# Performance work log

Hardware: AMD Instinct MI355X
Metric: run time of the kernel (lower is better)

Reference implementation:

```python
import jax, jax.numpy as jnp
import numpy as np

N, L, D, H = 4, 2048, 1024, 16
HD = D // H  # head_dim = 64


def setup_inputs() -> dict:
    key = jax.random.key(0)
    ks = jax.random.split(key, 6)
    x = jax.random.normal(ks[0], (N, L, D), dtype=jnp.float32)
    mask = jax.random.randint(ks[1], (N, L), 0, 2).astype(bool)
    W_qkv = jax.random.normal(ks[2], (3 * D, D), dtype=jnp.float32) * (1.0 / np.sqrt(D))
    b_qkv = jax.random.normal(ks[3], (3 * D,), dtype=jnp.float32) * 0.02
    W_out = jax.random.normal(ks[4], (D, D), dtype=jnp.float32) * (1.0 / np.sqrt(D))
    b_out = jax.random.normal(ks[5], (D,), dtype=jnp.float32) * 0.02
    return {"x": x, "mask": mask, "W_qkv": W_qkv, "b_qkv": b_qkv,
            "W_out": W_out, "b_out": b_out}


def reference(x, mask, W_qkv, b_qkv, W_out, b_out):
    # qkv projection: torch Linear is y = x @ W.T + b
    qkv = jnp.einsum('nld,ed->nle', x, W_qkv) + b_qkv          # [N, L, 3D]
    q, k, v = jnp.split(qkv, 3, axis=-1)                        # each [N, L, D]
    # [N, L, D] -> [N, H, L, HD]
    to_heads = lambda t: t.reshape(N, L, H, HD).transpose(0, 2, 1, 3)
    q, k, v = to_heads(q), to_heads(k), to_heads(v)
    scale = 1.0 / np.sqrt(HD)
    scores = jnp.einsum('nhqd,nhkd->nhqk', q, k) * scale        # [N, H, L, L]
    # faithful to source: masked_fill where mask is True -> -1e9
    scores = jnp.where(mask[:, None, None, :], -1e9, scores)
    attn = jax.nn.softmax(scores, axis=-1)                      # dropout = identity (eval)
    out = jnp.einsum('nhqk,nhkd->nhqd', attn, v)                # [N, H, L, HD]
    out = out.transpose(0, 2, 1, 3).reshape(N, L, D)
    return jnp.einsum('nld,ed->nle', out, W_out) + b_out
```

## Files before the change

### kernel.cpp

```cpp
#include <hip/hip_runtime.h>
#include <hip/hip_bf16.h>
#include <cmath>

#define NB   4
#define LL   2048
#define DD   1024
#define HH   16
#define HD   64

typedef __bf16 bf16;
typedef __bf16 bf16x4 __attribute__((ext_vector_type(4)));
typedef __bf16 bf16x8 __attribute__((ext_vector_type(8)));
typedef float  f32x4  __attribute__((ext_vector_type(4)));
typedef float  f32x8  __attribute__((ext_vector_type(8)));

__device__ __forceinline__ void gload16(void* lds_base, const void* gsrc) {
    __builtin_amdgcn_global_load_lds(
        (const __attribute__((address_space(1))) unsigned int*)gsrc,
        (__attribute__((address_space(3))) unsigned int*)lds_base, 16, 0, 0);
}

__global__ __launch_bounds__(1024) void mask_prep(const unsigned char* __restrict__ mraw,
                                                  float* __restrict__ maskB) {
    __shared__ int anyOdd;
    if (threadIdx.x == 0) anyOdd = 0;
    __syncthreads();
    const int base = blockIdx.x * 1024;
    const int i = base + threadIdx.x;
    if ((i & 3) != 0 && mraw[i] != 0) atomicOr(&anyOdd, 1);
    __syncthreads();
    const bool isBytes = (anyOdd != 0);
    int v = isBytes ? (int)mraw[i] : ((const int*)mraw)[i];
    maskB[i] = v ? -1.4426950408889634e9f : -12.0f;
}

__global__ __launch_bounds__(256) void cast_f32_bf16(const float* __restrict__ src,
                                                     bf16* __restrict__ dst, int n8) {
    const int i = blockIdx.x * 256 + threadIdx.x;
    if (i >= n8) return;
    const float4* s = (const float4*)src + (size_t)i * 2;
    float4 a = s[0], b = s[1];
    bf16x8 o;
    o[0] = (bf16)a.x; o[1] = (bf16)a.y; o[2] = (bf16)a.z; o[3] = (bf16)a.w;
    o[4] = (bf16)b.x; o[5] = (bf16)b.y; o[6] = (bf16)b.z; o[7] = (bf16)b.w;
    *((bf16x8*)dst + i) = o;
}

template <int EPI>
__global__ __launch_bounds__(256) void gemm_mfma(const bf16* __restrict__ A,
                                                 const bf16* __restrict__ B,
                                                 const float* __restrict__ bias,
                                                 void* __restrict__ C0v,
                                                 void* __restrict__ C1v,
                                                 void* __restrict__ C2v,
                                                 int M, int N, int K) {
    __shared__ __attribute__((aligned(16))) char As0[8192];
    __shared__ __attribute__((aligned(16))) char As1[8192];
    __shared__ __attribute__((aligned(16))) char Bs0[8192];
    __shared__ __attribute__((aligned(16))) char Bs1[8192];

    const int tid = threadIdx.x;
    const int wave = tid >> 6;
    const int lane = tid & 63;
    const int kl = lane & 15;
    const int h = lane >> 4;
    const int wm = wave >> 1;
    const int wn = wave & 1;
    const int m0 = blockIdx.y * 128;
    const int n0 = blockIdx.x * 128;

    f32x4 acc[4][4];
#pragma unroll
    for (int i = 0; i < 4; ++i)
#pragma unroll
        for (int j = 0; j < 4; ++j) acc[i][j] = (f32x4){0.f, 0.f, 0.f, 0.f};

    const int sr = wave * 16 + (lane >> 2);
    const int sc = (lane & 3) * 16;
    const char* A0 = (const char*)A + ((size_t)(m0 + sr) * K) * 2 + sc;
    const char* A1 = (const char*)A + ((size_t)(m0 + 64 + sr) * K) * 2 + sc;
    const char* B0 = (const char*)B + ((size_t)(n0 + sr) * K) * 2 + sc;
    const char* B1 = (const char*)B + ((size_t)(n0 + 64 + sr) * K) * 2 + sc;
    const int wofs = wave * 1024;

#define GSTAGE(AS, BS, kt)                          \
    do {                                            \
        gload16((AS) + wofs,        A0 + (kt) * 2); \
        gload16((AS) + wofs + 4096, A1 + (kt) * 2); \
        gload16((BS) + wofs,        B0 + (kt) * 2); \
        gload16((BS) + wofs + 4096, B1 + (kt) * 2); \
    } while (0)

#define GCOMPUTE(AS, BS)                                                           \
    do {                                                                           \
        bf16x8 a[4], b[4];                                                         \
        _Pragma("unroll") for (int mt = 0; mt < 4; ++mt)                           \
            a[mt] = *(const bf16x8*)((AS) + (wm * 64 + mt * 16 + kl) * 64 + h * 16); \
        _Pragma("unroll") for (int nt = 0; nt < 4; ++nt)                           \
            b[nt] = *(const bf16x8*)((BS) + (wn * 64 + nt * 16 + kl) * 64 + h * 16); \
        _Pragma("unroll") for (int mt = 0; mt < 4; ++mt)                           \
            _Pragma("unroll") for (int nt = 0; nt < 4; ++nt)                       \
                acc[mt][nt] = __builtin_amdgcn_mfma_f32_16x16x32_bf16(             \
                    a[mt], b[nt], acc[mt][nt], 0, 0, 0);                           \
    } while (0)

    GSTAGE(As0, Bs0, 0);
    asm volatile("s_waitcnt vmcnt(0)" ::: "memory");
    __builtin_amdgcn_s_barrier();

    for (int t = 0; t < 32; t += 2) {
        GSTAGE(As1, Bs1, (t + 1) * 32);
        __builtin_amdgcn_sched_barrier(0);
        GCOMPUTE(As0, Bs0);
        asm volatile("s_waitcnt vmcnt(0)" ::: "memory");
        __builtin_amdgcn_s_barrier();
        if (t + 2 < 32) {
            GSTAGE(As0, Bs0, (t + 2) * 32);
            __builtin_amdgcn_sched_barrier(0);
            GCOMPUTE(As1, Bs1);
            asm volatile("s_waitcnt vmcnt(0)" ::: "memory");
            __builtin_amdgcn_s_barrier();
        } else {
            GCOMPUTE(As1, Bs1);
        }
    }
#undef GSTAGE
#undef GCOMPUTE

    if (EPI == 1) {
        float* C0 = (float*)C0v;
#pragma unroll
        for (int mt = 0; mt < 4; ++mt) {
            const int mb = m0 + wm * 64 + mt * 16 + 4 * h;
#pragma unroll
            for (int nt = 0; nt < 4; ++nt) {
                const int n = n0 + wn * 64 + nt * 16 + kl;
                const float bv = bias[n];
#pragma unroll
                for (int r = 0; r < 4; ++r)
                    C0[(size_t)(mb + r) * N + n] = acc[mt][nt][r] + bv;
            }
        }
    } else {
        const int which = n0 >> 10;
        if (which < 2) {
            bf16* dst = (which == 0) ? (bf16*)C0v : (bf16*)C1v;
#pragma unroll
            for (int mt = 0; mt < 4; ++mt) {
                const int mb = m0 + wm * 64 + mt * 16 + 4 * h;
#pragma unroll
                for (int nt = 0; nt < 4; ++nt) {
                    const int gn = n0 + wn * 64 + nt * 16 + kl;
                    const float bv = bias[gn];
                    const int nn = gn & 1023;
                    const int hh = nn >> 6;
                    const int d = nn & 63;
#pragma unroll
                    for (int r = 0; r < 4; ++r) {
                        const int m = mb + r;
                        const int n_ = m >> 11;
                        const int l_ = m & 2047;
                        dst[((size_t)(n_ * HH + hh) * LL + l_) * HD + d] = (bf16)(acc[mt][nt][r] + bv);
                    }
                }
            }
        } else {
            bf16* dst = (bf16*)C2v;
#pragma unroll
            for (int mt = 0; mt < 4; ++mt) {
                const int mb = m0 + wm * 64 + mt * 16 + 4 * h;
                const int n_ = mb >> 11;
                const int l0 = mb & 2047;
#pragma unroll
                for (int nt = 0; nt < 4; ++nt) {
                    const int gn = n0 + wn * 64 + nt * 16 + kl;
                    const float bv = bias[gn];
                    const int nn = gn & 1023;
                    const int hh = nn >> 6;
                    const int d = nn & 63;
                    bf16x4 o4;
#pragma unroll
                    for (int r = 0; r < 4; ++r) o4[r] = (bf16)(acc[mt][nt][r] + bv);
                    *(bf16x4*)(dst + ((size_t)(n_ * HH + hh) * HD + d) * LL + l0) = o4;
                }
            }
        }
    }
}

#define SWZ3(row) ((((row) & 3) | ((((row) >> 3) & 1) << 2)) << 4)

__global__ __launch_bounds__(512) void attn_mfma(const bf16* __restrict__ Qg,
                                                 const bf16* __restrict__ Kg,
                                                 const bf16* __restrict__ VTg,
                                                 const float* __restrict__ maskB,
                                                 bf16* __restrict__ Oout) {
    __shared__ __attribute__((aligned(16))) char KtB0[8192];
    __shared__ __attribute__((aligned(16))) char KtB1[8192];
    __shared__ __attribute__((aligned(16))) char VtB0[8192];
    __shared__ __attribute__((aligned(16))) char VtB1[8192];

    const int tid = threadIdx.x;
    const int wave = tid >> 6;
    const int lane = tid & 63;
    const int kl = lane & 15;
    const int h = lane >> 4;

    const int f = blockIdx.x;
    const int qb = (f >> 3) & 7;
    const int bh = (f & 7) | ((f >> 6) << 3);
    const int n_ = bh >> 4;
    const int hh = bh & 15;
    const int q0 = qb * 256 + wave * 32;

    bf16x8 qf[2][2];
#pragma unroll
    for (int qt = 0; qt < 2; ++qt)
#pragma unroll
        for (int st = 0; st < 2; ++st)
            qf[qt][st] = *(const bf16x8*)(Qg + (((size_t)bh * LL + q0 + qt * 16 + kl) * HD + st * 32 + h * 8));

    f32x4 Oa[2][4];
    f32x4 Osum[2];
#pragma unroll
    for (int qt = 0; qt < 2; ++qt) {
        Osum[qt] = (f32x4){0.f, 0.f, 0.f, 0.f};
#pragma unroll
        for (int t = 0; t < 4; ++t) Oa[qt][t] = (f32x4){0.f, 0.f, 0.f, 0.f};
    }

    bf16x8 ones;
#pragma unroll
    for (int j = 0; j < 8; ++j) ones[j] = (bf16)1.0f;

    int koff[2][2][2];
#pragma unroll
    for (int c = 0; c < 2; ++c) {
        const int r1 = c * 32 + ((kl >> 2) << 3) + (kl & 3);
        const int r2 = r1 + 4;
#pragma unroll
        for (int st = 0; st < 2; ++st) {
            koff[c][0][st] = r1 * 128 + ((st * 64 + h * 16) ^ SWZ3(r1));
            koff[c][1][st] = r2 * 128 + ((st * 64 + h * 16) ^ SWZ3(r2));
        }
    }
    int voff[2][4];
#pragma unroll
    for (int c = 0; c < 2; ++c)
#pragma unroll
        for (int tt = 0; tt < 4; ++tt) {
            const int row = tt * 16 + kl;
            voff[c][tt] = row * 128 + ((c * 64 + h * 16) ^ SWZ3(row));
        }

    const int rA = wave * 8 + (lane >> 3);
    const int swA = ((lane & 7) << 4) ^ SWZ3(rA);
    const char* Kb = (const char*)Kg + (size_t)bh * LL * 128;
    const char* Vb = (const char*)VTg + (size_t)bh * HD * (LL * 2);
    const char* kSA = Kb + (size_t)rA * 128 + swA;
    const char* vSA = Vb + (size_t)rA * 4096 + swA;

    const float* mptr = maskB + n_ * LL + h * 8;
    const float scale = 0.18033688011f;

#define STAGE_TO(KT, VT, k0s)                                   \
    do {                                                        \
        gload16((KT) + wave * 1024, kSA + (size_t)(k0s) * 128); \
        gload16((VT) + wave * 1024, vSA + (k0s) * 2);           \
    } while (0)

#define LOADMK(MK, k0s)                                                      \
    do {                                                                     \
        _Pragma("unroll") for (int c = 0; c < 2; ++c)                        \
            _Pragma("unroll") for (int f2 = 0; f2 < 2; ++f2)                 \
                MK[c][f2] = *(const f32x4*)(mptr + (k0s) + c * 32 + f2 * 4); \
    } while (0)

#define COMPUTE(KT, VT, MK)                                                            \
    do {                                                                               \
        bf16x8 kf[2][2][2], vf[2][4];                                                  \
        _Pragma("unroll") for (int c = 0; c < 2; ++c)                                  \
            _Pragma("unroll") for (int fr = 0; fr < 2; ++fr)                           \
                _Pragma("unroll") for (int st = 0; st < 2; ++st)                       \
                    kf[c][fr][st] = *(const bf16x8*)((KT) + koff[c][fr][st]);          \
        __builtin_amdgcn_sched_barrier(0);             \
        _Pragma("unroll") for (int c = 0; c < 2; ++c)                                  \
            _Pragma("unroll") for (int tt = 0; tt < 4; ++tt)                           \
                vf[c][tt] = *(const bf16x8*)((VT) + voff[c][tt]);                      \
        asm volatile("s_waitcnt lgkmcnt(8)" ::: "memory");                \
        __builtin_amdgcn_sched_barrier(0);                                             \
        bf16x8 pa[2][2];                                                               \
        _Pragma("unroll") for (int qt = 0; qt < 2; ++qt) {                             \
            f32x4 sv[2][2];                                                            \
            _Pragma("unroll") for (int c = 0; c < 2; ++c)                              \
                _Pragma("unroll") for (int fr = 0; fr < 2; ++fr) {                     \
                    f32x4 z = {0.f, 0.f, 0.f, 0.f};                                    \
                    f32x4 a = __builtin_amdgcn_mfma_f32_16x16x32_bf16(kf[c][fr][0],    \
                                                         qf[qt][0], z, 0, 0, 0);       \
                    sv[c][fr] = __builtin_amdgcn_mfma_f32_16x16x32_bf16(kf[c][fr][1],  \
                                                         qf[qt][1], a, 0, 0, 0);       \
                }                                                                      \
            _Pragma("unroll") for (int c = 0; c < 2; ++c) {                            \
                f32x8 pf;                                                              \
                _Pragma("unroll") for (int f2 = 0; f2 < 2; ++f2) {                     \
                    f32x4 s = sv[c][f2] * scale + MK[c][f2];                           \
                    _Pragma("unroll") for (int r = 0; r < 4; ++r)                      \
                        pf[f2 * 4 + r] = __builtin_amdgcn_exp2f(s[r]);                 \
                }                                                                      \
                pa[qt][c] = __builtin_convertvector(pf, bf16x8);                       \
            }                                                                          \
        }                                                                              \
        asm volatile("s_waitcnt lgkmcnt(0)" ::: "memory");                \
        __builtin_amdgcn_sched_barrier(0);                                             \
        _Pragma("unroll") for (int qt = 0; qt < 2; ++qt) {                             \
            Osum[qt] = __builtin_amdgcn_mfma_f32_16x16x32_bf16(pa[qt][0], ones,        \
                                                               Osum[qt], 0, 0, 0);     \
            Osum[qt] = __builtin_amdgcn_mfma_f32_16x16x32_bf16(pa[qt][1], ones,        \
                                                               Osum[qt], 0, 0, 0);     \
            _Pragma("unroll") for (int c = 0; c < 2; ++c)                              \
                _Pragma("unroll") for (int tt = 0; tt < 4; ++tt)                       \
                    Oa[qt][tt] = __builtin_amdgcn_mfma_f32_16x16x32_bf16(pa[qt][c],    \
                                                 vf[c][tt], Oa[qt][tt], 0, 0, 0);      \
        }                                                                              \
    } while (0)

    f32x4 mkA[2][2], mkB[2][2];

    LOADMK(mkA, 0);
    STAGE_TO(KtB0, VtB0, 0);
    asm volatile("s_waitcnt vmcnt(0)" ::: "memory");
    __builtin_amdgcn_s_barrier();

    for (int t = 0; t < 32; t += 2) {
        STAGE_TO(KtB1, VtB1, (t + 1) * 64);
        __builtin_amdgcn_sched_barrier(0);
        LOADMK(mkB, (t + 1) * 64);
        COMPUTE(KtB0, VtB0, mkA);
        asm volatile("s_waitcnt vmcnt(4)" ::: "memory");
        __builtin_amdgcn_s_barrier();

        if (t + 2 < 32) {
            STAGE_TO(KtB0, VtB0, (t + 2) * 64);
            __builtin_amdgcn_sched_barrier(0);
            LOADMK(mkA, (t + 2) * 64);
            COMPUTE(KtB1, VtB1, mkB);
            asm volatile("s_waitcnt vmcnt(4)" ::: "memory");
            __builtin_amdgcn_s_barrier();
        } else {
            COMPUTE(KtB1, VtB1, mkB);
        }
    }

#pragma unroll
    for (int qt = 0; qt < 2; ++qt) {
#pragma unroll
        for (int r = 0; r < 4; ++r) {
            const float inv = 1.0f / Osum[qt][r];
            const int qrow = q0 + qt * 16 + h * 4 + r;
#pragma unroll
            for (int tt = 0; tt < 4; ++tt)
                Oout[((size_t)n_ * LL + qrow) * DD + hh * HD + tt * 16 + kl] =
                    (bf16)(Oa[qt][tt][r] * inv);
        }
    }
#undef STAGE_TO
#undef LOADMK
#undef COMPUTE
}

extern "C" void kernel_launch(void* const* d_in, const int* in_sizes, int n_in,
                              void* d_out, int out_size, void* d_ws, size_t ws_size,
                              hipStream_t stream) {
    const float* x     = (const float*)d_in[0];
    const void*  mask  = d_in[1];
    const float* W_qkv = (const float*)d_in[2];
    const float* b_qkv = (const float*)d_in[3];
    const float* W_out = (const float*)d_in[4];
    const float* b_out = (const float*)d_in[5];
    float* out = (float*)d_out;

    char* ws = (char*)d_ws;
    float* maskB = (float*)ws;
    bf16*  xb    = (bf16*)(ws + (1ull  << 20));
    bf16*  wqb   = (bf16*)(ws + (18ull << 20));
    bf16*  wob   = (bf16*)(ws + (25ull << 20));
    bf16*  qb    = (bf16*)(ws + (28ull << 20));
    bf16*  kb    = (bf16*)(ws + (45ull << 20));
    bf16*  vtb   = (bf16*)(ws + (62ull << 20));
    bf16*  attnb = (bf16*)(ws + (79ull << 20));

    mask_prep<<<8, 1024, 0, stream>>>((const unsigned char*)mask, maskB);

    cast_f32_bf16<<<(NB * LL * DD / 8) / 256, 256, 0, stream>>>(x, xb, NB * LL * DD / 8);
    cast_f32_bf16<<<(3 * DD * DD / 8) / 256, 256, 0, stream>>>(W_qkv, wqb, 3 * DD * DD / 8);
    cast_f32_bf16<<<(DD * DD / 8) / 256, 256, 0, stream>>>(W_out, wob, DD * DD / 8);

    gemm_mfma<0><<<dim3(3 * DD / 128, NB * LL / 128), 256, 0, stream>>>(
        xb, wqb, b_qkv, qb, kb, vtb, NB * LL, 3 * DD, DD);

    attn_mfma<<<512, 512, 0, stream>>>(qb, kb, vtb, maskB, attnb);

    gemm_mfma<1><<<dim3(DD / 128, NB * LL / 128), 256, 0, stream>>>(
        attnb, wob, b_out, out, nullptr, nullptr, NB * LL, DD, DD);
}
```

Baseline: 202.9 us.

## Load attention K/V fragments directly from global memory instead of LDS staging

Removes the double-buffered LDS staging of K and V tiles, along with its async global-to-LDS loads, swizzled offsets and per-tile block barriers. Each wave now reads its K/V MFMA fragments and mask values straight from global memory every iteration. This drops the synchronisation and LDS traffic, but each of the 8 waves in a block now fetches the same K/V tile on its own. Those uncoalesced, redundant global/L2 reads can leave the MFMA pipeline waiting on memory.

```diff
diff --git a/kernel.cpp b/kernel.cpp
--- a/kernel.cpp
+++ b/kernel.cpp
@@ -188,18 +188,11 @@
     }
 }
 
-#define SWZ3(row) ((((row) & 3) | ((((row) >> 3) & 1) << 2)) << 4)
-
 __global__ __launch_bounds__(512) void attn_mfma(const bf16* __restrict__ Qg,
                                                  const bf16* __restrict__ Kg,
                                                  const bf16* __restrict__ VTg,
                                                  const float* __restrict__ maskB,
                                                  bf16* __restrict__ Oout) {
-    __shared__ __attribute__((aligned(16))) char KtB0[8192];
-    __shared__ __attribute__((aligned(16))) char KtB1[8192];
-    __shared__ __attribute__((aligned(16))) char VtB0[8192];
-    __shared__ __attribute__((aligned(16))) char VtB1[8192];
-
     const int tid = threadIdx.x;
     const int wave = tid >> 6;
     const int lane = tid & 63;
@@ -233,121 +226,84 @@
 #pragma unroll
     for (int j = 0; j < 8; ++j) ones[j] = (bf16)1.0f;
 
-    int koff[2][2][2];
+    const char* Kb = (const char*)Kg + (size_t)bh * LL * 128;
+    const char* Vb = (const char*)VTg + (size_t)bh * HD * (LL * 2);
+    const char* kba[2][2][2];
 #pragma unroll
     for (int c = 0; c < 2; ++c) {
         const int r1 = c * 32 + ((kl >> 2) << 3) + (kl & 3);
-        const int r2 = r1 + 4;
-#pragma unroll
-        for (int st = 0; st < 2; ++st) {
-            koff[c][0][st] = r1 * 128 + ((st * 64 + h * 16) ^ SWZ3(r1));
-            koff[c][1][st] = r2 * 128 + ((st * 64 + h * 16) ^ SWZ3(r2));
-        }
-    }
-    int voff[2][4];
+#pragma unroll
+        for (int fr = 0; fr < 2; ++fr)
+#pragma unroll
+            for (int st = 0; st < 2; ++st)
+                kba[c][fr][st] = Kb + (r1 + 4 * fr) * 128 + st * 64 + h * 16;
+    }
+    const char* vba[2][4];
 #pragma unroll
     for (int c = 0; c < 2; ++c)
 #pragma unroll
-        for (int tt = 0; tt < 4; ++tt) {
-            const int row = tt * 16 + kl;
-            voff[c][tt] = row * 128 + ((c * 64 + h * 16) ^ SWZ3(row));
-        }
-
-    const int rA = wave * 8 + (lane >> 3);
-    const int swA = ((lane & 7) << 4) ^ SWZ3(rA);
-    const char* Kb = (const char*)Kg + (size_t)bh * LL * 128;
-    const char* Vb = (const char*)VTg + (size_t)bh * HD * (LL * 2);
-    const char* kSA = Kb + (size_t)rA * 128 + swA;
-    const char* vSA = Vb + (size_t)rA * 4096 + swA;
+        for (int tt = 0; tt < 4; ++tt)
+            vba[c][tt] = Vb + (tt * 16 + kl) * 4096 + (c * 32 + h * 8) * 2;
 
     const float* mptr = maskB + n_ * LL + h * 8;
     const float scale = 0.18033688011f;
 
-#define STAGE_TO(KT, VT, k0s)                                   \
-    do {                                                        \
-        gload16((KT) + wave * 1024, kSA + (size_t)(k0s) * 128); \
-        gload16((VT) + wave * 1024, vSA + (k0s) * 2);           \
-    } while (0)
-
-#define LOADMK(MK, k0s)                                                      \
-    do {                                                                     \
-        _Pragma("unroll") for (int c = 0; c < 2; ++c)                        \
-            _Pragma("unroll") for (int f2 = 0; f2 < 2; ++f2)                 \
-                MK[c][f2] = *(const f32x4*)(mptr + (k0s) + c * 32 + f2 * 4); \
-    } while (0)
-
-#define COMPUTE(KT, VT, MK)                                                            \
-    do {                                                                               \
-        bf16x8 kf[2][2][2], vf[2][4];                                                  \
-        _Pragma("unroll") for (int c = 0; c < 2; ++c)                                  \
-            _Pragma("unroll") for (int fr = 0; fr < 2; ++fr)                           \
-                _Pragma("unroll") for (int st = 0; st < 2; ++st)                       \
-                    kf[c][fr][st] = *(const bf16x8*)((KT) + koff[c][fr][st]);          \
-        __builtin_amdgcn_sched_barrier(0);             \
-        _Pragma("unroll") for (int c = 0; c < 2; ++c)                                  \
-            _Pragma("unroll") for (int tt = 0; tt < 4; ++tt)                           \
-                vf[c][tt] = *(const bf16x8*)((VT) + voff[c][tt]);                      \
-        asm volatile("s_waitcnt lgkmcnt(8)" ::: "memory");                \
-        __builtin_amdgcn_sched_barrier(0);                                             \
-        bf16x8 pa[2][2];                                                               \
-        _Pragma("unroll") for (int qt = 0; qt < 2; ++qt) {                             \
-            f32x4 sv[2][2];                                                            \
-            _Pragma("unroll") for (int c = 0; c < 2; ++c)                              \
-                _Pragma("unroll") for (int fr = 0; fr < 2; ++fr) {                     \
-                    f32x4 z = {0.f, 0.f, 0.f, 0.f};                                    \
-                    f32x4 a = __builtin_amdgcn_mfma_f32_16x16x32_bf16(kf[c][fr][0],    \
-                                                         qf[qt][0], z, 0, 0, 0);       \
-                    sv[c][fr] = __builtin_amdgcn_mfma_f32_16x16x32_bf16(kf[c][fr][1],  \
-                                                         qf[qt][1], a, 0, 0, 0);       \
-                }                                                                      \
-            _Pragma("unroll") for (int c = 0; c < 2; ++c) {                            \
-                f32x8 pf;                                                              \
-                _Pragma("unroll") for (int f2 = 0; f2 < 2; ++f2) {                     \
-                    f32x4 s = sv[c][f2] * scale + MK[c][f2];                           \
-                    _Pragma("unroll") for (int r = 0; r < 4; ++r)                      \
-                        pf[f2 * 4 + r] = __builtin_amdgcn_exp2f(s[r]);                 \
-                }                                                                      \
-                pa[qt][c] = __builtin_convertvector(pf, bf16x8);                       \
-            }                                                                          \
-        }                                                                              \
-        asm volatile("s_waitcnt lgkmcnt(0)" ::: "memory");                \
-        __builtin_amdgcn_sched_barrier(0);                                             \
-        _Pragma("unroll") for (int qt = 0; qt < 2; ++qt) {                             \
-            Osum[qt] = __builtin_amdgcn_mfma_f32_16x16x32_bf16(pa[qt][0], ones,        \
-                                                               Osum[qt], 0, 0, 0);     \
-            Osum[qt] = __builtin_amdgcn_mfma_f32_16x16x32_bf16(pa[qt][1], ones,        \
-                                                               Osum[qt], 0, 0, 0);     \
-            _Pragma("unroll") for (int c = 0; c < 2; ++c)                              \
-                _Pragma("unroll") for (int tt = 0; tt < 4; ++tt)                       \
-                    Oa[qt][tt] = __builtin_amdgcn_mfma_f32_16x16x32_bf16(pa[qt][c],    \
-                                                 vf[c][tt], Oa[qt][tt], 0, 0, 0);      \
-        }                                                                              \
-    } while (0)
-
-    f32x4 mkA[2][2], mkB[2][2];
-
-    LOADMK(mkA, 0);
-    STAGE_TO(KtB0, VtB0, 0);
-    asm volatile("s_waitcnt vmcnt(0)" ::: "memory");
-    __builtin_amdgcn_s_barrier();
-
-    for (int t = 0; t < 32; t += 2) {
-        STAGE_TO(KtB1, VtB1, (t + 1) * 64);
-        __builtin_amdgcn_sched_barrier(0);
-        LOADMK(mkB, (t + 1) * 64);
-        COMPUTE(KtB0, VtB0, mkA);
-        asm volatile("s_waitcnt vmcnt(4)" ::: "memory");
-        __builtin_amdgcn_s_barrier();
-
-        if (t + 2 < 32) {
-            STAGE_TO(KtB0, VtB0, (t + 2) * 64);
-            __builtin_amdgcn_sched_barrier(0);
-            LOADMK(mkA, (t + 2) * 64);
-            COMPUTE(KtB1, VtB1, mkB);
-            asm volatile("s_waitcnt vmcnt(4)" ::: "memory");
-            __builtin_amdgcn_s_barrier();
-        } else {
-            COMPUTE(KtB1, VtB1, mkB);
+    for (int t = 0; t < 32; ++t) {
+        const int k0 = t * 64;
+
+        bf16x8 kf[2][2][2], vf[2][4];
+#pragma unroll
+        for (int c = 0; c < 2; ++c) {
+#pragma unroll
+            for (int fr = 0; fr < 2; ++fr)
+#pragma unroll
+                for (int st = 0; st < 2; ++st)
+                    kf[c][fr][st] = *(const bf16x8*)(kba[c][fr][st] + (size_t)k0 * 128);
+#pragma unroll
+            for (int tt = 0; tt < 4; ++tt)
+                vf[c][tt] = *(const bf16x8*)(vba[c][tt] + k0 * 2);
+        }
+        f32x4 mk[2][2];
+#pragma unroll
+        for (int c = 0; c < 2; ++c)
+#pragma unroll
+            for (int f2 = 0; f2 < 2; ++f2)
+                mk[c][f2] = *(const f32x4*)(mptr + k0 + c * 32 + f2 * 4);
+
+        bf16x8 pa[2][2];
+#pragma unroll
+        for (int qt = 0; qt < 2; ++qt) {
+            f32x4 sv[2][2];
+#pragma unroll
+            for (int c = 0; c < 2; ++c)
+#pragma unroll
+                for (int fr = 0; fr < 2; ++fr) {
+                    f32x4 z = {0.f, 0.f, 0.f, 0.f};
+                    f32x4 a = __builtin_amdgcn_mfma_f32_16x16x32_bf16(kf[c][fr][0], qf[qt][0], z, 0, 0, 0);
+                    sv[c][fr] = __builtin_amdgcn_mfma_f32_16x16x32_bf16(kf[c][fr][1], qf[qt][1], a, 0, 0, 0);
+                }
+#pragma unroll
+            for (int c = 0; c < 2; ++c) {
+                f32x8 pf;
+#pragma unroll
+                for (int f2 = 0; f2 < 2; ++f2) {
+                    f32x4 s = sv[c][f2] * scale + mk[c][f2];
+#pragma unroll
+                    for (int r = 0; r < 4; ++r)
+                        pf[f2 * 4 + r] = __builtin_amdgcn_exp2f(s[r]);
+                }
+                pa[qt][c] = __builtin_convertvector(pf, bf16x8);
+            }
+        }
+#pragma unroll
+        for (int qt = 0; qt < 2; ++qt) {
+            Osum[qt] = __builtin_amdgcn_mfma_f32_16x16x32_bf16(pa[qt][0], ones, Osum[qt], 0, 0, 0);
+            Osum[qt] = __builtin_amdgcn_mfma_f32_16x16x32_bf16(pa[qt][1], ones, Osum[qt], 0, 0, 0);
+#pragma unroll
+            for (int c = 0; c < 2; ++c)
+#pragma unroll
+                for (int tt = 0; tt < 4; ++tt)
+                    Oa[qt][tt] = __builtin_amdgcn_mfma_f32_16x16x32_bf16(pa[qt][c], vf[c][tt], Oa[qt][tt], 0, 0, 0);
         }
     }
 
@@ -363,9 +319,6 @@
                     (bf16)(Oa[qt][tt][r] * inv);
         }
     }
-#undef STAGE_TO
-#undef LOADMK
-#undef COMPUTE
 }
 
 extern "C" void kernel_launch(void* const* d_in, const int* in_sizes, int n_in,
```

Result: slower. 363.4 us (+79.1%).

## Stage 128-key tiles per barrier and preload mask row into LDS

Applied to the files above, without the earlier changes.

The attention loop now stages two 64-key K/V tiles per pipeline step, which halves the number of barriers and loop iterations. The full mask row for the batch is loaded into LDS once at the start, replacing per-tile global mask loads with LDS reads inside COMPUTE. This raises LDS use from 32KB to 72KB per block, which may cut occupancy. It also waits with vmcnt(0) instead of vmcnt(4), so prefetch overlap is slightly weaker.

```diff
diff --git a/kernel.cpp b/kernel.cpp
--- a/kernel.cpp
+++ b/kernel.cpp
@@ -195,10 +195,11 @@
                                                  const bf16* __restrict__ VTg,
                                                  const float* __restrict__ maskB,
                                                  bf16* __restrict__ Oout) {
-    __shared__ __attribute__((aligned(16))) char KtB0[8192];
-    __shared__ __attribute__((aligned(16))) char KtB1[8192];
-    __shared__ __attribute__((aligned(16))) char VtB0[8192];
-    __shared__ __attribute__((aligned(16))) char VtB1[8192];
+    __shared__ __attribute__((aligned(16))) char K0A[8192], K1A[8192];
+    __shared__ __attribute__((aligned(16))) char V0A[8192], V1A[8192];
+    __shared__ __attribute__((aligned(16))) char K0B[8192], K1B[8192];
+    __shared__ __attribute__((aligned(16))) char V0B[8192], V1B[8192];
+    __shared__ __attribute__((aligned(16))) char MaskL[8192];
 
     const int tid = threadIdx.x;
     const int wave = tid >> 6;
@@ -260,34 +261,33 @@
     const char* kSA = Kb + (size_t)rA * 128 + swA;
     const char* vSA = Vb + (size_t)rA * 4096 + swA;
 
-    const float* mptr = maskB + n_ * LL + h * 8;
     const float scale = 0.18033688011f;
-
-#define STAGE_TO(KT, VT, k0s)                                   \
-    do {                                                        \
-        gload16((KT) + wave * 1024, kSA + (size_t)(k0s) * 128); \
-        gload16((VT) + wave * 1024, vSA + (k0s) * 2);           \
+    const char* mlds = MaskL + h * 32;
+
+#define STAGE4(K0T, K1T, V0T, V1T, k0s)                            \
+    do {                                                           \
+        gload16((K0T) + wave * 1024, kSA + (size_t)(k0s) * 128);   \
+        gload16((K1T) + wave * 1024, kSA + (size_t)((k0s) + 64) * 128); \
+        gload16((V0T) + wave * 1024, vSA + (k0s) * 2);             \
+        gload16((V1T) + wave * 1024, vSA + ((k0s) + 64) * 2);      \
     } while (0)
 
-#define LOADMK(MK, k0s)                                                      \
-    do {                                                                     \
-        _Pragma("unroll") for (int c = 0; c < 2; ++c)                        \
-            _Pragma("unroll") for (int f2 = 0; f2 < 2; ++f2)                 \
-                MK[c][f2] = *(const f32x4*)(mptr + (k0s) + c * 32 + f2 * 4); \
-    } while (0)
-
-#define COMPUTE(KT, VT, MK)                                                            \
+#define COMPUTE(KT, VT, MB)                                                            \
     do {                                                                               \
+        f32x4 mk[2][2];                                                                \
+        _Pragma("unroll") for (int c = 0; c < 2; ++c)                                  \
+            _Pragma("unroll") for (int f2 = 0; f2 < 2; ++f2)                           \
+                mk[c][f2] = *(const f32x4*)(mlds + (MB) + c * 128 + f2 * 16);          \
         bf16x8 kf[2][2][2], vf[2][4];                                                  \
         _Pragma("unroll") for (int c = 0; c < 2; ++c)                                  \
             _Pragma("unroll") for (int fr = 0; fr < 2; ++fr)                           \
                 _Pragma("unroll") for (int st = 0; st < 2; ++st)                       \
                     kf[c][fr][st] = *(const bf16x8*)((KT) + koff[c][fr][st]);          \
-        __builtin_amdgcn_sched_barrier(0);             \
+        __builtin_amdgcn_sched_barrier(0);              \
         _Pragma("unroll") for (int c = 0; c < 2; ++c)                                  \
             _Pragma("unroll") for (int tt = 0; tt < 4; ++tt)                           \
                 vf[c][tt] = *(const bf16x8*)((VT) + voff[c][tt]);                      \
-        asm volatile("s_waitcnt lgkmcnt(8)" ::: "memory");                \
+        asm volatile("s_waitcnt lgkmcnt(8)" ::: "memory");           \
         __builtin_amdgcn_sched_barrier(0);                                             \
         bf16x8 pa[2][2];                                                               \
         _Pragma("unroll") for (int qt = 0; qt < 2; ++qt) {                             \
@@ -303,7 +303,7 @@
             _Pragma("unroll") for (int c = 0; c < 2; ++c) {                            \
                 f32x8 pf;                                                              \
                 _Pragma("unroll") for (int f2 = 0; f2 < 2; ++f2) {                     \
-                    f32x4 s = sv[c][f2] * scale + MK[c][f2];                           \
+                    f32x4 s = sv[c][f2] * scale + mk[c][f2];                           \
                     _Pragma("unroll") for (int r = 0; r < 4; ++r)                      \
                         pf[f2 * 4 + r] = __builtin_amdgcn_exp2f(s[r]);                 \
                 }                                                                      \
@@ -324,30 +324,32 @@
         }                                                                              \
     } while (0)
 
-    f32x4 mkA[2][2], mkB[2][2];
-
-    LOADMK(mkA, 0);
-    STAGE_TO(KtB0, VtB0, 0);
+    {
+        const char* msrc = (const char*)(maskB + n_ * LL) + wave * 1024 + lane * 16;
+        gload16(MaskL + wave * 1024, msrc);
+    }
+    STAGE4(K0A, K1A, V0A, V1A, 0);
     asm volatile("s_waitcnt vmcnt(0)" ::: "memory");
     __builtin_amdgcn_s_barrier();
 
-    for (int t = 0; t < 32; t += 2) {
-        STAGE_TO(KtB1, VtB1, (t + 1) * 64);
+    for (int t = 0; t < 16; t += 2) {
+        STAGE4(K0B, K1B, V0B, V1B, (t + 1) * 128);
         __builtin_amdgcn_sched_barrier(0);
-        LOADMK(mkB, (t + 1) * 64);
-        COMPUTE(KtB0, VtB0, mkA);
-        asm volatile("s_waitcnt vmcnt(4)" ::: "memory");
+        COMPUTE(K0A, V0A, t * 512);
+        COMPUTE(K1A, V1A, t * 512 + 256);
+        asm volatile("s_waitcnt vmcnt(0)" ::: "memory");
         __builtin_amdgcn_s_barrier();
 
-        if (t + 2 < 32) {
-            STAGE_TO(KtB0, VtB0, (t + 2) * 64);
+        if (t + 2 < 16) {
+            STAGE4(K0A, K1A, V0A, V1A, (t + 2) * 128);
             __builtin_amdgcn_sched_barrier(0);
-            LOADMK(mkA, (t + 2) * 64);
-            COMPUTE(KtB1, VtB1, mkB);
-            asm volatile("s_waitcnt vmcnt(4)" ::: "memory");
+            COMPUTE(K0B, V0B, (t + 1) * 512);
+            COMPUTE(K1B, V1B, (t + 1) * 512 + 256);
+            asm volatile("s_waitcnt vmcnt(0)" ::: "memory");
             __builtin_amdgcn_s_barrier();
         } else {
-            COMPUTE(KtB1, VtB1, mkB);
+            COMPUTE(K0B, V0B, (t + 1) * 512);
+            COMPUTE(K1B, V1B, (t + 1) * 512 + 256);
         }
     }
 
@@ -363,8 +365,7 @@
                     (bf16)(Oa[qt][tt][r] * inv);
         }
     }
-#undef STAGE_TO
-#undef LOADMK
+#undef STAGE4
 #undef COMPUTE
 }
 
```

After: 195.0 us. 1.04x faster.
